# Kernel optimization log

Measured on AMD Instinct MI355X. Metric: run time of the kernel, lower is better.

Reference implementation:

```python
import jax, jax.numpy as jnp
import numpy as np

B, T, IDIM, HDIM, K, LMAX, NLAYERS = 64, 1024, 120, 320, 72, 96, 3
LAMB = 0.1
NEG = -1e30


def lse3(a, b, c):
    m = jnp.maximum(jnp.maximum(a, b), c)
    return m + jnp.log(jnp.exp(a - m) + jnp.exp(b - m) + jnp.exp(c - m))


def _lstm_dir(x, Wih, Whh, bb):
    # x: [B,T,D] -> h: [B,T,H]; PyTorch gate order i,f,g,o
    gx = jnp.einsum('btd,gd->tbg', x, Wih) + bb  # [T,B,4H]
    def step(carry, g):
        h, c = carry
        g = g + h @ Whh.T
        i, f, gg, o = jnp.split(g, 4, axis=-1)
        c = jax.nn.sigmoid(f) * c + jax.nn.sigmoid(i) * jnp.tanh(gg)
        h = jax.nn.sigmoid(o) * jnp.tanh(c)
        return (h, c), h
    h0 = jnp.zeros((x.shape[0], HDIM), x.dtype)
    _, hs = jax.lax.scan(step, (h0, h0), gx)
    return hs.transpose(1, 0, 2)


def _rev(x, lengths):
    # reverse each sequence within its valid length (packed-sequence semantics)
    t = jnp.arange(x.shape[1])
    idx = jnp.where(t[None, :] < lengths[:, None], lengths[:, None] - 1 - t[None, :], t[None, :])
    return jnp.take_along_axis(x, idx[:, :, None], axis=1)


def _blstm_layer(x, Wih_f, Whh_f, b_f, Wih_b, Whh_b, b_b, lengths):
    hf = _lstm_dir(x, Wih_f, Whh_f, b_f)
    hb = _rev(_lstm_dir(_rev(x, lengths), Wih_b, Whh_b, b_b), lengths)
    return jnp.concatenate([hf, hb], axis=2)


def _ctc_forward(logp, labels, in_lens, lab_lens):
    # standard CTC alpha recursion (blank=0), log-space, vectorized over batch
    Bn, Tn, _ = logp.shape
    S = 2 * LMAX + 1
    ext = jnp.zeros((Bn, S), jnp.int32).at[:, 1::2].set(labels)  # blank-interleaved labels
    em = jnp.take_along_axis(logp, jnp.broadcast_to(ext[:, None, :], (Bn, Tn, S)), axis=2)
    em = em.transpose(1, 0, 2)  # [T,B,S]
    s_idx = jnp.arange(S)
    prev_lab = jnp.concatenate([jnp.full((Bn, 2), -1, jnp.int32), ext[:, :-2]], axis=1)
    can_skip = ((s_idx[None, :] % 2) == 1) & (ext != prev_lab)
    valid_s = s_idx[None, :] < (2 * lab_lens[:, None] + 1)
    alpha0 = jnp.full((Bn, S), NEG, logp.dtype)
    alpha0 = alpha0.at[:, 0].set(em[0][:, 0]).at[:, 1].set(em[0][:, 1])
    alpha0 = jnp.where(valid_s, alpha0, NEG)
    def step(alpha, inp):
        em_t, t = inp
        a2 = jnp.concatenate([jnp.full((Bn, 1), NEG, alpha.dtype), alpha[:, :-1]], axis=1)
        a3 = jnp.concatenate([jnp.full((Bn, 2), NEG, alpha.dtype), alpha[:, :-2]], axis=1)
        a3 = jnp.where(can_skip, a3, NEG)
        new = lse3(alpha, a2, a3) + em_t
        new = jnp.where(valid_s, new, NEG)
        new = jnp.where((t < in_lens)[:, None], new, alpha)  # freeze past utterance end
        return new, None
    alpha, _ = jax.lax.scan(step, alpha0, (em[1:], jnp.arange(1, Tn)))
    last = 2 * lab_lens
    aL = jnp.take_along_axis(alpha, last[:, None], axis=1)[:, 0]
    aLm1 = jnp.take_along_axis(alpha, (last - 1)[:, None], axis=1)[:, 0]
    return jnp.logaddexp(aL, aLm1)  # log p(labels | x)


def setup_inputs():
    key = jax.random.key(0)
    ks = jax.random.split(key, 12)
    H4 = 4 * HDIM
    s = 0.05
    return dict(
        logits=jax.random.normal(ks[0], (B, T, IDIM), jnp.float32),
        labels_padded=jax.random.randint(ks[1], (B, LMAX), 1, K).astype(jnp.int32),
        input_lengths=jax.random.randint(ks[2], (B,), T // 2, T + 1).astype(jnp.int32),
        label_lengths=jax.random.randint(ks[3], (B,), LMAX // 2, LMAX + 1).astype(jnp.int32),
        Wih0=jax.random.normal(ks[4], (2, H4, IDIM), jnp.float32) * s,
        Whh0=jax.random.normal(ks[5], (2, H4, HDIM), jnp.float32) * s,
        b0=jnp.zeros((2, H4), jnp.float32),
        Wih=jax.random.normal(ks[6], (NLAYERS - 1, 2, H4, 2 * HDIM), jnp.float32) * s,
        Whh=jax.random.normal(ks[7], (NLAYERS - 1, 2, H4, HDIM), jnp.float32) * s,
        b=jnp.zeros((NLAYERS - 1, 2, H4), jnp.float32),
        W_lin=jax.random.normal(ks[8], (K, 2 * HDIM), jnp.float32) * s,
        b_lin=jnp.zeros((K,), jnp.float32),
    )


def reference(logits, labels_padded, input_lengths, label_lengths, Wih0, Whh0, b0, Wih, Whh, b, W_lin, b_lin):
    # sort by input length descending (mirrors torch.sort + index_select)
    order = jnp.argsort(-input_lengths)
    logits = logits[order]
    labels_padded = labels_padded[order]
    input_lengths = input_lengths[order]
    label_lengths = label_lengths[order]
    # 3-layer BLSTM encoder
    x = _blstm_layer(logits, Wih0[0], Whh0[0], b0[0], Wih0[1], Whh0[1], b0[1], input_lengths)
    for l in range(NLAYERS - 1):
        x = _blstm_layer(x, Wih[l, 0], Whh[l, 0], b[l, 0], Wih[l, 1], Whh[l, 1], b[l, 1], input_lengths)
    netout = jax.nn.log_softmax(x @ W_lin.T + b_lin, axis=2)  # [B,T,K]
    # CTC-CRF: numerator = CTC alpha log-prob; denominator = free-running partition
    num = _ctc_forward(netout, labels_padded, input_lengths, label_lengths)
    tmask = jnp.arange(netout.shape[1])[None, :] < input_lengths[:, None]
    den = jnp.sum(jnp.where(tmask, jax.nn.logsumexp(netout, axis=2), 0.0), axis=1)
    return jnp.mean(den - (1.0 + LAMB) * num)
```

## Files before the change

### kernel.cpp

```cpp
#include <hip/hip_runtime.h>
#include <cstdint>
#include <cstddef>


typedef _Float16 f16;
typedef _Float16 h2v   __attribute__((ext_vector_type(2)));
typedef _Float16 f16x4v __attribute__((ext_vector_type(4)));
typedef _Float16 f16x8 __attribute__((ext_vector_type(8)));
typedef float    f32x4 __attribute__((ext_vector_type(4)));
typedef uint32_t u32x4 __attribute__((ext_vector_type(4)));

#define NEGF (-1e30f)
#define CT 128

__device__ __forceinline__ int dot4i8(int a, int b, int c) {
#if __has_builtin(__builtin_amdgcn_sdot4)
  return __builtin_amdgcn_sdot4(a, b, c, false);
#else
  int s = c;
#pragma unroll
  for (int e = 0; e < 4; ++e)
    s += (int)(int8_t)(a >> (8 * e)) * (int)(int8_t)(b >> (8 * e));
  return s;
#endif
}

__device__ __forceinline__ float fast_rcp(float x) {
#if __has_builtin(__builtin_amdgcn_rcpf)
  return __builtin_amdgcn_rcpf(x);
#else
  return 1.f / x;
#endif
}
__device__ __forceinline__ float fsigm(float x) { return fast_rcp(1.f + __expf(-x)); }
__device__ __forceinline__ float ftanh(float x) { return 1.f - 2.f * fast_rcp(1.f + __expf(2.f * x)); }

__device__ __forceinline__ float fexp2(float x) {
#if __has_builtin(__builtin_amdgcn_exp2f)
  return __builtin_amdgcn_exp2f(x);
#else
  return exp2f(x);
#endif
}
__device__ __forceinline__ float flog2(float x) {
#if __has_builtin(__builtin_amdgcn_logf)
  return __builtin_amdgcn_logf(x);
#else
  return log2f(x);
#endif
}

__device__ __forceinline__ void stage16(f16* lds, const f16* g) {
#if __has_builtin(__builtin_amdgcn_global_load_lds)
  __builtin_amdgcn_global_load_lds(
      (const __attribute__((address_space(1))) uint32_t*)g,
      (__attribute__((address_space(3))) uint32_t*)lds, 16, 0, 0);
#else
  int lane = threadIdx.x & 63;
  *(f16x8*)&lds[lane * 8] = *(const f16x8*)g;
#endif
}


__global__ void conv_logits(const float* __restrict__ src, f16* __restrict__ dst) {
  int idx = blockIdx.x * 256 + threadIdx.x;
  int row = idx >> 7, k = idx & 127;
  dst[idx] = (f16)((k < 120) ? src[(size_t)row * 120 + k] : 0.f);
}

__global__ void conv_wt0(const float* __restrict__ w, f16* __restrict__ dst) {
  int idx = blockIdx.x * 256 + threadIdx.x;
  int n = idx >> 7, k = idx & 127;
  dst[idx] = (f16)((k < 120) ? w[(size_t)n * 120 + k] : 0.f);
}

__global__ void conv_copy(const float* __restrict__ src, f16* __restrict__ dst, int count) {
  int idx = blockIdx.x * 256 + threadIdx.x;
  if (idx < count) dst[idx] = (f16)src[idx];
}

__global__ void conv_wtl(const float* __restrict__ w, f16* __restrict__ dst) {
  int idx = blockIdx.x * 256 + threadIdx.x;
  int n = idx / 640, k = idx % 640;
  dst[idx] = (f16)((n < 72) ? w[(size_t)n * 640 + k] : 0.f);
}

__global__ void conv_scale(const float* __restrict__ whh0, const float* __restrict__ whh,
                           float* __restrict__ scales) {
  int row = blockIdx.x * 4 + (threadIdx.x >> 6);
  int lane = threadIdx.x & 63;
  int slot = row / 1280, r = row - slot * 1280;
  const float* src = (slot < 2) ? (whh0 + ((size_t)slot * 1280 + r) * 320)
                                : (whh  + ((size_t)(slot - 2) * 1280 + r) * 320);
  float m = 0.f;
  for (int k = lane; k < 320; k += 64) m = fmaxf(m, fabsf(src[k]));
#pragma unroll
  for (int o = 32; o; o >>= 1) m = fmaxf(m, __shfl_xor(m, o, 64));
  if (lane == 0) scales[row] = fmaxf(m, 1e-20f) * (1.f / 127.f);
}

__global__ void conv_wq(const float* __restrict__ whh0, const float* __restrict__ whh,
                        const float* __restrict__ scales, uint32_t* __restrict__ dst) {
  int o = blockIdx.x * 256 + threadIdx.x;
  int t = o & 511;
  int g = o >> 9;
  int j = g % 20;
  int g2 = g / 20;
  int i = g2 % 10;
  int slot = g2 / 10;
  int qi = t >> 2, kq = t & 3;
  int r = i * 128 + qi;
  int k0 = kq * 80 + j * 4;
  const float* src = (slot < 2) ? (whh0 + ((size_t)slot * 1280 + r) * 320)
                                : (whh  + ((size_t)(slot - 2) * 1280 + r) * 320);
  float s = scales[slot * 1280 + r];
  float rs = fast_rcp(s);
  uint32_t w = 0;
#pragma unroll
  for (int e = 0; e < 4; ++e) {
    float q = rintf(src[k0 + e] * rs);
    q = fminf(fmaxf(q, -127.f), 127.f);
    w |= ((uint32_t)(uint8_t)(int8_t)(int)q) << (8 * e);
  }
  dst[o] = w;
}

__global__ __launch_bounds__(256)
void gemm_chunk(const f16* __restrict__ A, const f16* __restrict__ W,
                f16* __restrict__ gxc, const int* __restrict__ lens,
                int lda, int kTiles, int c0) {
  __shared__ __align__(16) f16 As[128 * 32];
  __shared__ __align__(16) f16 Ws[2][128 * 32];
  const int tid = threadIdx.x;
  const int lane = tid & 63, wid = tid >> 6;
  const int wm = wid >> 1, wn = wid & 1;
  const int dir = blockIdx.y >> 6, b = blockIdx.y & 63;
  const int n0 = blockIdx.x * 256;
  const int r_base = lane >> 2;
  const int chs = ((((lane & 3) + (r_base >> 1)) & 3)) * 8;
  const int len = lens[b];

  f32x4 acc[4][8] = {};

  for (int kt = 0; kt < kTiles; ++kt) {
    const int k0 = kt * 32;
    __syncthreads();
#pragma unroll
    for (int hh = 0; hh < 2; ++hh) {
      const int c = wid * 2 + hh;
      const int j = c * 16 + r_base;
      const int s = c0 * CT + j;
      const int tt = dir ? ((s < len) ? (len - 1 - s) : s) : s;
      stage16(&As[c * 512], A + (size_t)(b * 1024 + tt) * lda + k0 + chs);
    }
#pragma unroll
    for (int hh = 0; hh < 4; ++hh) {
      const int c = wid * 4 + hh;
      const int tile = c >> 3, cc = c & 7;
      stage16(&Ws[tile][cc * 512],
              W + (size_t)(dir * 1280 + n0 + tile * 128 + cc * 16 + r_base) * lda + k0 + chs);
    }
    __syncthreads();

    const int q = lane >> 4;
    const int l15 = lane & 15;
    const int cs = (q - (l15 >> 1)) & 3;
    const int rofs = l15 * 32 + cs * 8;
    f16x8 av[4], wv0[4], wv1[4];
#pragma unroll
    for (int i = 0; i < 4; ++i)
      av[i] = *(const f16x8*)&As[(wm * 4 + i) * 512 + rofs];
#pragma unroll
    for (int i = 0; i < 4; ++i) {
      wv0[i] = *(const f16x8*)&Ws[0][(wn * 4 + i) * 512 + rofs];
      wv1[i] = *(const f16x8*)&Ws[1][(wn * 4 + i) * 512 + rofs];
    }
#pragma unroll
    for (int i = 0; i < 4; ++i)
#pragma unroll
      for (int j = 0; j < 4; ++j) {
        acc[i][j]     = __builtin_amdgcn_mfma_f32_16x16x32_f16(av[i], wv0[j], acc[i][j], 0, 0, 0);
        acc[i][4 + j] = __builtin_amdgcn_mfma_f32_16x16x32_f16(av[i], wv1[j], acc[i][4 + j], 0, 0, 0);
      }
  }

  const int r0 = (lane >> 4) * 4, cn = lane & 15;
  const size_t obase = (size_t)(dir * 64 + b) * CT;
#pragma unroll
  for (int i = 0; i < 4; ++i) {
    const int m = wm * 64 + i * 16 + r0;
#pragma unroll
    for (int j = 0; j < 4; ++j) {
      const int n = n0 + wn * 64 + j * 16 + cn;
#pragma unroll
      for (int r = 0; r < 4; ++r) {
        gxc[(obase + m + r) * 1280 + n]       = (f16)acc[i][j][r];
        gxc[(obase + m + r) * 1280 + n + 128] = (f16)acc[i][4 + j][r];
      }
    }
  }
}

__global__ void __launch_bounds__(512)
__attribute__((amdgpu_waves_per_eu(2, 2)))
lstm_scan_chunk(const uint32_t* __restrict__ wqbuf,
                const float* __restrict__ scales,
                const f16* __restrict__ gxc,
                const float* __restrict__ bias,
                const int* __restrict__ lens,
                f16* __restrict__ xnext,
                f16* __restrict__ hsave,
                float* __restrict__ csave,
                int layer, int c0) {
  const int wg = blockIdx.x;
  const int b = wg >> 1, dir = wg & 1;
  const int tid = threadIdx.x;
  const int kq = tid & 3, qi = tid >> 2;
  const int slot = layer * 2 + dir;

  __shared__ __align__(16) uint32_t hqw[80];
  __shared__ int ylds[1280];
  __shared__ float bsl[1280];
  __shared__ float ssl[1280];
  __shared__ __align__(16) f16 hstage[112 * 320];

  uint32_t w[10][20];
  {
    const uint32_t* wb = wqbuf + (size_t)slot * 10 * 20 * 512;
#pragma unroll
    for (int i = 0; i < 10; ++i)
#pragma unroll
      for (int j = 0; j < 20; ++j)
        w[i][j] = wb[(i * 20 + j) * 512 + tid];
  }

  for (int v = tid; v < 1280; v += 512) {
    bsl[v] = bias[dir * 1280 + v];
    ssl[v] = scales[slot * 1280 + v] * (1.f / 127.f);
  }

  const int len = lens[b];
  float c_state = 0.f;
  if (tid < 320) {
    float hv0 = (c0 == 0) ? 0.f : (float)hsave[wg * 320 + tid];
    ((uint8_t*)hqw)[tid] = (uint8_t)(int8_t)(int)rintf(hv0 * 127.f);
    if (c0 > 0) c_state = csave[wg * 320 + tid];
  }
  __syncthreads();

  const size_t grow0 = (size_t)(dir * 64 + b) * CT;

  float gxi = 0.f, gxf = 0.f, gxg = 0.f, gxo = 0.f;
  if (tid < 320) {
    const f16* gp = gxc + grow0 * 1280 + tid;
    gxi = (float)gp[0]; gxf = (float)gp[320]; gxg = (float)gp[640]; gxo = (float)gp[960];
  }

  for (int tl = 0; tl < CT; ++tl) {
    float nxi = 0.f, nxf = 0.f, nxg = 0.f, nxo = 0.f;
    if (tid < 320 && tl + 1 < CT) {
      const f16* gp = gxc + (grow0 + tl + 1) * 1280 + tid;
      nxi = (float)gp[0]; nxf = (float)gp[320]; nxg = (float)gp[640]; nxo = (float)gp[960];
    }

    int acc0 = 0, acc1 = 0, acc2 = 0, acc3 = 0, acc4 = 0;
    int acc5 = 0, acc6 = 0, acc7 = 0, acc8 = 0, acc9 = 0;
    {
      const u32x4* hv4 = (const u32x4*)&hqw[kq * 20];
#pragma unroll
      for (int jb = 0; jb < 5; ++jb) {
        u32x4 hv = hv4[jb];
#pragma unroll
        for (int e = 0; e < 4; ++e) {
          const int j = jb * 4 + e;
          const int hword = (int)hv[e];
          acc0 = dot4i8((int)w[0][j], hword, acc0);
          acc1 = dot4i8((int)w[1][j], hword, acc1);
          acc2 = dot4i8((int)w[2][j], hword, acc2);
          acc3 = dot4i8((int)w[3][j], hword, acc3);
          acc4 = dot4i8((int)w[4][j], hword, acc4);
          acc5 = dot4i8((int)w[5][j], hword, acc5);
          acc6 = dot4i8((int)w[6][j], hword, acc6);
          acc7 = dot4i8((int)w[7][j], hword, acc7);
          acc8 = dot4i8((int)w[8][j], hword, acc8);
          acc9 = dot4i8((int)w[9][j], hword, acc9);
        }
      }
    }
    {
      int av[10] = {acc0, acc1, acc2, acc3, acc4, acc5, acc6, acc7, acc8, acc9};
#pragma unroll
      for (int i = 0; i < 10; ++i) {
        int v = av[i];
        v += __shfl_xor(v, 1, 64);
        v += __shfl_xor(v, 2, 64);
        if (kq == 0) ylds[i * 128 + qi] = v;
      }
    }

    if ((tl & 31) == 0 && tl > 0) {
      const int tw = tl - 32;
#pragma unroll
      for (int it = 0; it < 3; ++it) {
        const int slt = it * 512 + tid;
        if (slt < 1280) {
          const int r = (int)(((unsigned)slt * 1639u) >> 16);
          const int j = slt - r * 40;
          const int sp = c0 * CT + tw + r;
          const int ttp = dir ? ((sp < len) ? (len - 1 - sp) : sp) : sp;
          f16x8 v = *(const f16x8*)&hstage[((tw + r) & 63) * 320 + j * 8];
          *(f16x8*)&xnext[(size_t)(b * 1024 + ttp) * 640 + dir * 320 + j * 8] = v;
        }
      }
    }
    __syncthreads();

    if (tid < 320) {
      const int u = tid;
      float pi = ssl[u]       * (float)ylds[u]       + gxi + bsl[u];
      float pf = ssl[u + 320] * (float)ylds[u + 320] + gxf + bsl[u + 320];
      float pg = ssl[u + 640] * (float)ylds[u + 640] + gxg + bsl[u + 640];
      float po = ssl[u + 960] * (float)ylds[u + 960] + gxo + bsl[u + 960];
      float ig = fsigm(pi);
      float fg = fsigm(pf);
      float gg = ftanh(pg);
      float og = fsigm(po);
      c_state = fg * c_state + ig * gg;
      float hv = og * ftanh(c_state);
      hstage[(tl & 63) * 320 + u] = (f16)hv;
      ((uint8_t*)hqw)[u] = (uint8_t)(int8_t)(int)rintf(hv * 127.f);
    }
    __syncthreads();

    gxi = nxi; gxf = nxf; gxg = nxg; gxo = nxo;
  }

  {
    const int tw = CT - 32;
#pragma unroll
    for (int it = 0; it < 3; ++it) {
      const int slt = it * 512 + tid;
      if (slt < 1280) {
        const int r = (int)(((unsigned)slt * 1639u) >> 16);
        const int j = slt - r * 40;
        const int sp = c0 * CT + tw + r;
        const int ttp = dir ? ((sp < len) ? (len - 1 - sp) : sp) : sp;
        f16x8 v = *(const f16x8*)&hstage[((tw + r) & 63) * 320 + j * 8];
        *(f16x8*)&xnext[(size_t)(b * 1024 + ttp) * 640 + dir * 320 + j * 8] = v;
      }
    }
  }
  if (tid < 320) {
    hsave[wg * 320 + tid] = hstage[63 * 320 + tid];
    csave[wg * 320 + tid] = c_state;
  }
}

__global__ __launch_bounds__(256)
void gemm_proj(const f16* __restrict__ A, const f16* __restrict__ W,
               float* __restrict__ outf, int lda, int kTiles, int ldo) {
  __shared__ __align__(16) f16 As[128 * 32];
  __shared__ __align__(16) f16 Ws[128 * 32];
  const int tid = threadIdx.x;
  const int lane = tid & 63, wid = tid >> 6;
  const int wm = wid >> 1, wn = wid & 1;
  const int m0 = blockIdx.y * 128, n0 = blockIdx.x * 128;
  const int r_base = lane >> 2;
  const int chs = ((((lane & 3) + (r_base >> 1)) & 3)) * 8;

  f32x4 acc[4][4] = {};

  for (int kt = 0; kt < kTiles; ++kt) {
    const int k0 = kt * 32;
    __syncthreads();
#pragma unroll
    for (int hh = 0; hh < 2; ++hh) {
      const int c = wid * 2 + hh;
      stage16(&As[c * 512], A + (size_t)(m0 + c * 16 + r_base) * lda + k0 + chs);
      stage16(&Ws[c * 512], W + (size_t)(n0 + c * 16 + r_base) * lda + k0 + chs);
    }
    __syncthreads();

    const int q = lane >> 4;
    const int l15 = lane & 15;
    const int cs = (q - (l15 >> 1)) & 3;
    const int rofs = l15 * 32 + cs * 8;
    f16x8 av[4], wv[4];
#pragma unroll
    for (int i = 0; i < 4; ++i)
      av[i] = *(const f16x8*)&As[(wm * 4 + i) * 512 + rofs];
#pragma unroll
    for (int i = 0; i < 4; ++i)
      wv[i] = *(const f16x8*)&Ws[(wn * 4 + i) * 512 + rofs];
#pragma unroll
    for (int i = 0; i < 4; ++i)
#pragma unroll
      for (int j = 0; j < 4; ++j)
        acc[i][j] = __builtin_amdgcn_mfma_f32_16x16x32_f16(av[i], wv[j], acc[i][j], 0, 0, 0);
  }

  const int r0 = (lane >> 4) * 4, cn = lane & 15;
#pragma unroll
  for (int i = 0; i < 4; ++i) {
    const int m = m0 + wm * 64 + i * 16 + r0;
#pragma unroll
    for (int j = 0; j < 4; ++j) {
      const int n = n0 + wn * 64 + j * 16 + cn;
#pragma unroll
      for (int r = 0; r < 4; ++r)
        outf[(size_t)(m + r) * ldo + n] = acc[i][j][r];
    }
  }
}

__global__ void lse_kernel(const float* __restrict__ Z, const float* __restrict__ b_lin,
                           float* __restrict__ lseout) {
  int row = blockIdx.x * 4 + (threadIdx.x >> 6);
  int l = threadIdx.x & 63;
  const float* z = Z + (size_t)row * 128;
  float v0 = (l < 72) ? z[l] + b_lin[l] : NEGF;
  float v1 = (l < 8) ? z[l + 64] + b_lin[l + 64] : NEGF;
  float m = fmaxf(v0, v1);
#pragma unroll
  for (int o = 32; o; o >>= 1) m = fmaxf(m, __shfl_xor(m, o, 64));
  float s = ((l < 72) ? __expf(v0 - m) : 0.f) + ((l < 8) ? __expf(v1 - m) : 0.f);
#pragma unroll
  for (int o = 32; o; o >>= 1) s += __shfl_xor(s, o, 64);
  if (l == 0) lseout[row] = m + __logf(s);
}

__global__ void emz_kernel(const float* __restrict__ Z, const float* __restrict__ lse,
                           const float* __restrict__ b_lin,
                           const int* __restrict__ labels,
                           f16* __restrict__ emc) {
  const int b = blockIdx.y;
  const int t0 = blockIdx.x * 4;
  const int tid = threadIdx.x;
  __shared__ int ext[200];
  __shared__ float bls[200];
  if (tid < 200) {
    int e = (tid < 193 && (tid & 1)) ? labels[b * 96 + (tid >> 1)] : 0;
    ext[tid] = e;
    bls[tid] = b_lin[e];
  }
  __syncthreads();
#pragma unroll
  for (int dt = 0; dt < 4; ++dt) {
    const int t = t0 + dt;
    const float lst = lse[b * 1024 + t];
    const float* zr = Z + ((size_t)(b * 1024 + t)) * 128;
    for (int s = tid; s < 200; s += 256)
      emc[((size_t)(b * 1024 + t)) * 200 + s] =
          (f16)((zr[ext[s]] + bls[s] - lst) * 1.4426950408889634f);
  }
}

__global__ void ctc_kernel(const f16* __restrict__ emc,
                           const int* __restrict__ labels, const int* __restrict__ inlen,
                           const int* __restrict__ lablen, float* __restrict__ num) {
  const int b = blockIdx.x;
  const int lane = threadIdx.x;
  __shared__ int ext[200];
  __shared__ float afin[200];

  for (int s = lane; s < 200; s += 64)
    ext[s] = (s < 193 && (s & 1)) ? labels[b * 96 + (s >> 1)] : 0;
  __syncthreads();

  const int L = lablen[b], len = inlen[b];
  const int Send = 2 * L + 1;
  const f16* eb = emc + (size_t)b * 1024 * 200;

  float a[4];
  bool  skp[4], val[4];
#pragma unroll
  for (int j = 0; j < 4; ++j) {
    const int s = lane * 4 + j;
    val[j] = (s < Send) && (s < 193);
    skp[j] = (s < 193) && (s & 1) && (s >= 2) && (ext[s] != ext[s - 2]);
  }
  {
    f16x4v e0 = *(const f16x4v*)&eb[lane * 4];
#pragma unroll
    for (int j = 0; j < 4; ++j) {
      const int s = lane * 4 + j;
      a[j] = (s <= 1 && val[j]) ? (float)e0[j] : NEGF;
    }
  }

  auto step = [&](f16x4v ev) {
    float p3 = __shfl_up(a[3], 1, 64);
    float p2 = __shfl_up(a[2], 1, 64);
    if (lane == 0) { p3 = NEGF; p2 = NEGF; }
    const float x2[4] = {p3, a[0], a[1], a[2]};
    const float x3[4] = {p2, p3, a[0], a[1]};
#pragma unroll
    for (int j = 0; j < 4; ++j) {
      const float xa = a[j], xb = x2[j];
      const float xc = skp[j] ? x3[j] : NEGF;
      const float m = fmaxf(xa, fmaxf(xb, xc));
      const float sum = fexp2(xa - m) + fexp2(xb - m) + fexp2(xc - m);
      const float nv = m + flog2(sum) + (float)ev[j];
      a[j] = val[j] ? nv : NEGF;
    }
  };

  f16x4v ring[8];
#pragma unroll
  for (int d = 1; d <= 8; ++d) {
    const int r = (d < len) ? d : (len - 1);
    ring[d & 7] = *(const f16x4v*)&eb[(size_t)r * 200 + lane * 4];
  }

  int t = 1;
  for (; t + 8 <= len; t += 8) {
#pragma unroll
    for (int k = 0; k < 8; ++k) {
      const int slot = (1 + k) & 7;
      f16x4v ev = ring[slot];
      const int tp = t + k + 8;
      if (tp < len)
        ring[slot] = *(const f16x4v*)&eb[(size_t)tp * 200 + lane * 4];
      step(ev);
    }
  }
  for (; t < len; ++t)
    step(*(const f16x4v*)&eb[(size_t)t * 200 + lane * 4]);

#pragma unroll
  for (int j = 0; j < 4; ++j) {
    const int s = lane * 4 + j;
    if (s < 193) afin[s] = a[j];
  }
  __syncthreads();
  if (lane == 0) {
    const float aL = afin[2 * L], aLm1 = afin[2 * L - 1];
    const float m = fmaxf(aL, aLm1);
    num[b] = 0.6931471805599453f * (m + flog2(fexp2(aL - m) + fexp2(aLm1 - m)));
  }
}

__global__ void final_kernel(const float* __restrict__ num, float* __restrict__ out) {
  int l = threadIdx.x;
  float v = -1.1f * num[l];
#pragma unroll
  for (int o = 32; o; o >>= 1) v += __shfl_xor(v, o, 64);
  if (l == 0) out[0] = v * (1.f / 64.f);
}

__global__ void sentinel_kernel(float* __restrict__ out, float code) { out[0] = code; }

extern "C" void kernel_launch(void* const* d_in, const int* in_sizes, int n_in,
                              void* d_out, int out_size, void* d_ws, size_t ws_size,
                              hipStream_t stream) {
  (void)in_sizes; (void)n_in; (void)out_size;

  const float* logits   = (const float*)d_in[0];
  const int*   labels   = (const int*)d_in[1];
  const int*   in_lens  = (const int*)d_in[2];
  const int*   lab_lens = (const int*)d_in[3];
  const float* Wih0     = (const float*)d_in[4];
  const float* Whh0     = (const float*)d_in[5];
  const float* b0       = (const float*)d_in[6];
  const float* Wih      = (const float*)d_in[7];
  const float* Whh      = (const float*)d_in[8];
  const float* bb       = (const float*)d_in[9];
  const float* W_lin    = (const float*)d_in[10];
  const float* b_lin    = (const float*)d_in[11];

  const size_t NEED = (size_t)224 * 1024 * 1024;
  if (ws_size < NEED) {
    sentinel_kernel<<<1, 1, 0, stream>>>((float*)d_out, -(float)(ws_size >> 20));
    return;
  }

  char* ws = (char*)d_ws;
  size_t off = 0;
  auto alloc = [&](size_t bytes) -> char* {
    char* p = ws + off;
    off += (bytes + 255) & ~(size_t)255;
    return p;
  };
  f16*      Xa     = (f16*)alloc((size_t)65536 * 640 * 2);
  f16*      Xb     = (f16*)alloc((size_t)65536 * 640 * 2);
  f16*      gxc    = (f16*)alloc((size_t)2 * 64 * CT * 1280 * 2);
  f16*      Wt0    = (f16*)alloc((size_t)2560 * 128 * 2);
  f16*      Wt12   = (f16*)alloc((size_t)2 * 2560 * 640 * 2);
  f16*      WtL    = (f16*)alloc((size_t)128 * 640 * 2);
  uint32_t* wqi    = (uint32_t*)alloc((size_t)6 * 10 * 20 * 512 * 4);
  float*    scales = (float*)alloc((size_t)6 * 1280 * 4);
  float*    lseb   = (float*)alloc((size_t)65536 * 4);
  float*    num    = (float*)alloc(64 * 4);
  f16*      hsave  = (f16*)alloc((size_t)128 * 320 * 2);
  float*    csave  = (float*)alloc((size_t)128 * 320 * 4);
  f16*      A0     = Xb;
  float*    Z      = (float*)gxc;
  f16*      emc    = Xa;

  conv_logits<<<32768, 256, 0, stream>>>(logits, A0);
  conv_wt0<<<1280, 256, 0, stream>>>(Wih0, Wt0);
  conv_copy<<<12800, 256, 0, stream>>>(Wih, Wt12, 3276800);
  conv_wtl<<<320, 256, 0, stream>>>(W_lin, WtL);
  conv_scale<<<1920, 256, 0, stream>>>(Whh0, Whh, scales);
  conv_wq<<<2400, 256, 0, stream>>>(Whh0, Whh, scales, wqi);

  for (int c = 0; c < 1024 / CT; ++c) {
    gemm_chunk<<<dim3(5, 128), 256, 0, stream>>>(A0, Wt0, gxc, in_lens, 128, 4, c);
    lstm_scan_chunk<<<128, 512, 0, stream>>>(wqi, scales, gxc, b0, in_lens, Xa,
                                             hsave, csave, 0, c);
  }
  for (int c = 0; c < 1024 / CT; ++c) {
    gemm_chunk<<<dim3(5, 128), 256, 0, stream>>>(Xa, Wt12, gxc, in_lens, 640, 20, c);
    lstm_scan_chunk<<<128, 512, 0, stream>>>(wqi, scales, gxc, bb, in_lens, Xb,
                                             hsave, csave, 1, c);
  }
  for (int c = 0; c < 1024 / CT; ++c) {
    gemm_chunk<<<dim3(5, 128), 256, 0, stream>>>(Xb, Wt12 + (size_t)2560 * 640, gxc,
                                                 in_lens, 640, 20, c);
    lstm_scan_chunk<<<128, 512, 0, stream>>>(wqi, scales, gxc, bb + 2560, in_lens, Xa,
                                             hsave, csave, 2, c);
  }
  gemm_proj<<<dim3(1, 512), 256, 0, stream>>>(Xa, WtL, Z, 640, 20, 128);

  lse_kernel<<<16384, 256, 0, stream>>>(Z, b_lin, lseb);
  emz_kernel<<<dim3(256, 64), 256, 0, stream>>>(Z, lseb, b_lin, labels, emc);
  ctc_kernel<<<64, 64, 0, stream>>>(emc, labels, in_lens, lab_lens, num);
  final_kernel<<<1, 64, 0, stream>>>(num, (float*)d_out);
}
```

Baseline: 8.417 ms.

## Split recurrent weights across registers, LDS and streamed global loads in LSTM scan

The int8 recurrent weight matrix used to sit entirely in registers (200 VGPRs per thread). Now half stays in registers, three gate-row blocks go to LDS, and two are streamed from a repacked global buffer each timestep with one-block-ahead prefetch. To make LDS room, the h staging buffer shrinks from 112 rows to 8, with output flushed every 8 steps, and the fixed waves-per-EU attribute is dropped. This lowers register pressure but adds LDS and global/L2 traffic on the serial critical path of each timestep.

```diff
diff --git a/kernel.cpp b/kernel.cpp
--- a/kernel.cpp
+++ b/kernel.cpp
@@ -125,6 +125,18 @@
   dst[o] = w;
 }
 
+__global__ void conv_wqs(const uint32_t* __restrict__ wqi, uint32_t* __restrict__ wqs) {
+  int o = blockIdx.x * 256 + threadIdx.x;
+  int e = o & 3;
+  int t = (o >> 2) & 511;
+  int g = o >> 11;
+  int jb = g % 5;
+  int g2 = g / 5;
+  int ip = g2 & 1;
+  int slot = g2 >> 1;
+  wqs[o] = wqi[(size_t)slot * 102400 + ((8 + ip) * 20 + jb * 4 + e) * 512 + t];
+}
+
 __global__ __launch_bounds__(256)
 void gemm_chunk(const f16* __restrict__ A, const f16* __restrict__ W,
                 f16* __restrict__ gxc, const int* __restrict__ lens,
@@ -202,8 +214,8 @@
 }
 
 __global__ void __launch_bounds__(512)
-__attribute__((amdgpu_waves_per_eu(2, 2)))
 lstm_scan_chunk(const uint32_t* __restrict__ wqbuf,
+                const uint32_t* __restrict__ wqs,
                 const float* __restrict__ scales,
                 const f16* __restrict__ gxc,
                 const float* __restrict__ bias,
@@ -222,16 +234,24 @@
   __shared__ int ylds[1280];
   __shared__ float bsl[1280];
   __shared__ float ssl[1280];
-  __shared__ __align__(16) f16 hstage[112 * 320];
-
-  uint32_t w[10][20];
+  __shared__ __align__(16) uint32_t lw[3 * 5 * 512 * 4];
+  __shared__ __align__(16) f16 hstage[8 * 320];
+
+  uint32_t w[5][20];
   {
     const uint32_t* wb = wqbuf + (size_t)slot * 10 * 20 * 512;
 #pragma unroll
-    for (int i = 0; i < 10; ++i)
+    for (int i = 0; i < 5; ++i)
 #pragma unroll
       for (int j = 0; j < 20; ++j)
         w[i][j] = wb[(i * 20 + j) * 512 + tid];
+#pragma unroll
+    for (int ip2 = 0; ip2 < 3; ++ip2)
+#pragma unroll
+      for (int j = 0; j < 20; ++j) {
+        uint32_t v = wb[((5 + ip2) * 20 + j) * 512 + tid];
+        lw[(((ip2 * 5 + (j >> 2)) * 512 + tid) << 2) + (j & 3)] = v;
+      }
   }
 
   for (int v = tid; v < 1280; v += 512) {
@@ -249,6 +269,7 @@
   __syncthreads();
 
   const size_t grow0 = (size_t)(dir * 64 + b) * CT;
+  const u32x4* gs = (const u32x4*)wqs + (size_t)slot * 10 * 512;
 
   float gxi = 0.f, gxf = 0.f, gxg = 0.f, gxo = 0.f;
   if (tid < 320) {
@@ -267,9 +288,20 @@
     int acc5 = 0, acc6 = 0, acc7 = 0, acc8 = 0, acc9 = 0;
     {
       const u32x4* hv4 = (const u32x4*)&hqw[kq * 20];
+      const u32x4* lw4 = (const u32x4*)lw;
+      u32x4 ga = gs[0 * 512 + tid];
+      u32x4 gb = gs[5 * 512 + tid];
 #pragma unroll
       for (int jb = 0; jb < 5; ++jb) {
         u32x4 hv = hv4[jb];
+        u32x4 l0 = lw4[(0 * 5 + jb) * 512 + tid];
+        u32x4 l1 = lw4[(1 * 5 + jb) * 512 + tid];
+        u32x4 l2 = lw4[(2 * 5 + jb) * 512 + tid];
+        u32x4 ca = ga, cb = gb;
+        if (jb < 4) {
+          ga = gs[(0 * 5 + jb + 1) * 512 + tid];
+          gb = gs[(1 * 5 + jb + 1) * 512 + tid];
+        }
 #pragma unroll
         for (int e = 0; e < 4; ++e) {
           const int j = jb * 4 + e;
@@ -279,11 +311,11 @@
           acc2 = dot4i8((int)w[2][j], hword, acc2);
           acc3 = dot4i8((int)w[3][j], hword, acc3);
           acc4 = dot4i8((int)w[4][j], hword, acc4);
-          acc5 = dot4i8((int)w[5][j], hword, acc5);
-          acc6 = dot4i8((int)w[6][j], hword, acc6);
-          acc7 = dot4i8((int)w[7][j], hword, acc7);
-          acc8 = dot4i8((int)w[8][j], hword, acc8);
-          acc9 = dot4i8((int)w[9][j], hword, acc9);
+          acc5 = dot4i8((int)l0[e], hword, acc5);
+          acc6 = dot4i8((int)l1[e], hword, acc6);
+          acc7 = dot4i8((int)l2[e], hword, acc7);
+          acc8 = dot4i8((int)ca[e], hword, acc8);
+          acc9 = dot4i8((int)cb[e], hword, acc9);
         }
       }
     }
@@ -298,19 +330,15 @@
       }
     }
 
-    if ((tl & 31) == 0 && tl > 0) {
-      const int tw = tl - 32;
-#pragma unroll
-      for (int it = 0; it < 3; ++it) {
-        const int slt = it * 512 + tid;
-        if (slt < 1280) {
-          const int r = (int)(((unsigned)slt * 1639u) >> 16);
-          const int j = slt - r * 40;
-          const int sp = c0 * CT + tw + r;
-          const int ttp = dir ? ((sp < len) ? (len - 1 - sp) : sp) : sp;
-          f16x8 v = *(const f16x8*)&hstage[((tw + r) & 63) * 320 + j * 8];
-          *(f16x8*)&xnext[(size_t)(b * 1024 + ttp) * 640 + dir * 320 + j * 8] = v;
-        }
+    if ((tl & 7) == 0 && tl > 0) {
+      const int tw = tl - 8;
+      if (tid < 320) {
+        const int r = (int)(((unsigned)tid * 1639u) >> 16);
+        const int j = tid - r * 40;
+        const int sp = c0 * CT + tw + r;
+        const int ttp = dir ? ((sp < len) ? (len - 1 - sp) : sp) : sp;
+        f16x8 v = *(const f16x8*)&hstage[r * 320 + j * 8];
+        *(f16x8*)&xnext[(size_t)(b * 1024 + ttp) * 640 + dir * 320 + j * 8] = v;
       }
     }
     __syncthreads();
@@ -327,7 +355,7 @@
       float og = fsigm(po);
       c_state = fg * c_state + ig * gg;
       float hv = og * ftanh(c_state);
-      hstage[(tl & 63) * 320 + u] = (f16)hv;
+      hstage[(tl & 7) * 320 + u] = (f16)hv;
       ((uint8_t*)hqw)[u] = (uint8_t)(int8_t)(int)rintf(hv * 127.f);
     }
     __syncthreads();
@@ -336,22 +364,18 @@
   }
 
   {
-    const int tw = CT - 32;
-#pragma unroll
-    for (int it = 0; it < 3; ++it) {
-      const int slt = it * 512 + tid;
-      if (slt < 1280) {
-        const int r = (int)(((unsigned)slt * 1639u) >> 16);
-        const int j = slt - r * 40;
-        const int sp = c0 * CT + tw + r;
-        const int ttp = dir ? ((sp < len) ? (len - 1 - sp) : sp) : sp;
-        f16x8 v = *(const f16x8*)&hstage[((tw + r) & 63) * 320 + j * 8];
-        *(f16x8*)&xnext[(size_t)(b * 1024 + ttp) * 640 + dir * 320 + j * 8] = v;
-      }
+    const int tw = CT - 8;
+    if (tid < 320) {
+      const int r = (int)(((unsigned)tid * 1639u) >> 16);
+      const int j = tid - r * 40;
+      const int sp = c0 * CT + tw + r;
+      const int ttp = dir ? ((sp < len) ? (len - 1 - sp) : sp) : sp;
+      f16x8 v = *(const f16x8*)&hstage[r * 320 + j * 8];
+      *(f16x8*)&xnext[(size_t)(b * 1024 + ttp) * 640 + dir * 320 + j * 8] = v;
     }
   }
   if (tid < 320) {
-    hsave[wg * 320 + tid] = hstage[63 * 320 + tid];
+    hsave[wg * 320 + tid] = hstage[7 * 320 + tid];
     csave[wg * 320 + tid] = c_state;
   }
 }
@@ -588,6 +612,7 @@
   f16*      Wt12   = (f16*)alloc((size_t)2 * 2560 * 640 * 2);
   f16*      WtL    = (f16*)alloc((size_t)128 * 640 * 2);
   uint32_t* wqi    = (uint32_t*)alloc((size_t)6 * 10 * 20 * 512 * 4);
+  uint32_t* wqs    = (uint32_t*)alloc((size_t)6 * 2 * 5 * 512 * 4 * 4);
   float*    scales = (float*)alloc((size_t)6 * 1280 * 4);
   float*    lseb   = (float*)alloc((size_t)65536 * 4);
   float*    num    = (float*)alloc(64 * 4);
@@ -603,21 +628,22 @@
   conv_wtl<<<320, 256, 0, stream>>>(W_lin, WtL);
   conv_scale<<<1920, 256, 0, stream>>>(Whh0, Whh, scales);
   conv_wq<<<2400, 256, 0, stream>>>(Whh0, Whh, scales, wqi);
+  conv_wqs<<<480, 256, 0, stream>>>(wqi, wqs);
 
   for (int c = 0; c < 1024 / CT; ++c) {
     gemm_chunk<<<dim3(5, 128), 256, 0, stream>>>(A0, Wt0, gxc, in_lens, 128, 4, c);
-    lstm_scan_chunk<<<128, 512, 0, stream>>>(wqi, scales, gxc, b0, in_lens, Xa,
+    lstm_scan_chunk<<<128, 512, 0, stream>>>(wqi, wqs, scales, gxc, b0, in_lens, Xa,
                                              hsave, csave, 0, c);
   }
   for (int c = 0; c < 1024 / CT; ++c) {
     gemm_chunk<<<dim3(5, 128), 256, 0, stream>>>(Xa, Wt12, gxc, in_lens, 640, 20, c);
-    lstm_scan_chunk<<<128, 512, 0, stream>>>(wqi, scales, gxc, bb, in_lens, Xb,
+    lstm_scan_chunk<<<128, 512, 0, stream>>>(wqi, wqs, scales, gxc, bb, in_lens, Xb,
                                              hsave, csave, 1, c);
   }
   for (int c = 0; c < 1024 / CT; ++c) {
     gemm_chunk<<<dim3(5, 128), 256, 0, stream>>>(Xb, Wt12 + (size_t)2560 * 640, gxc,
                                                  in_lens, 640, 20, c);
-    lstm_scan_chunk<<<128, 512, 0, stream>>>(wqi, scales, gxc, bb + 2560, in_lens, Xa,
+    lstm_scan_chunk<<<128, 512, 0, stream>>>(wqi, wqs, scales, gxc, bb + 2560, in_lens, Xa,
                                              hsave, csave, 2, c);
   }
   gemm_proj<<<dim3(1, 512), 256, 0, stream>>>(Xa, WtL, Z, 640, 20, 128);
```

After: 9.031 ms. +7.3%, slower.
